# Performance work log

Hardware: AMD Instinct MI355X
Metric: run time of the kernel (lower is better)

Reference implementation:

```python
import jax, jax.numpy as jnp
import numpy as np

SIGMA = 0.02
B, CC, H, W = 4, 21, 96, 96
C_LOW, C_HIGH = 3, 512
N = H * W


def _grid_edges(h, w):
    idx = np.arange(h * w).reshape(h, w)
    eh = np.stack([idx[:, :-1].ravel(), idx[:, 1:].ravel()], 1)
    ev = np.stack([idx[:-1, :].ravel(), idx[1:, :].ravel()], 1)
    return np.concatenate([eh, ev], 0)  # [E,2] 4-connected grid edges


def _mst_bfs(feat, h, w):
    # feat: [C,h,w] numpy. Kruskal MST with norm2 edge weights, then BFS from node 0.
    n = h * w
    edges = _grid_edges(h, w)
    f = feat.reshape(feat.shape[0], -1)
    wts = ((f[:, edges[:, 0]] - f[:, edges[:, 1]]) ** 2).sum(0)
    order = np.argsort(wts, kind='stable')
    uf = np.arange(n)

    def find(x):
        r = x
        while uf[r] != r:
            r = uf[r]
        while uf[x] != r:
            uf[x], x = r, uf[x]
        return r

    adj = [[] for _ in range(n)]
    cnt = 0
    for ei in order:
        a, b = int(edges[ei, 0]), int(edges[ei, 1])
        ra, rb = find(a), find(b)
        if ra != rb:
            uf[ra] = rb
            adj[a].append(b)
            adj[b].append(a)
            cnt += 1
            if cnt == n - 1:
                break
    parent = np.zeros(n, np.int64)
    seen = np.zeros(n, bool)
    seen[0] = True
    levels, frontier = [[0]], [0]
    while frontier:
        nxt = []
        for u in frontier:
            for v in adj[u]:
                if not seen[v]:
                    seen[v] = True
                    parent[v] = u
                    nxt.append(v)
        if nxt:
            levels.append(nxt)
        frontier = nxt
    return parent, levels


def _tree_arrays(embed):
    # Host-side MST + BFS level schedule (integer tree topology, non-differentiable).
    e = np.asarray(jax.device_get(embed)).astype(np.float64)
    bn = e.shape[0]
    parents, levels = [], []
    for b in range(bn):
        p, lv = _mst_bfs(e[b], H, W)
        parents.append(p)
        levels.append(lv)
    D = max(len(lv) for lv in levels)
    L = max(max(len(l) for l in lv) for lv in levels)
    nodes = np.full((bn, D, L), N, np.int32)  # index N = dummy sink node
    for b, lv in enumerate(levels):
        for d, l in enumerate(lv):
            nodes[b, d, :len(l)] = l
    par = np.stack(parents)
    par = np.concatenate([par, np.full((bn, 1), N)], 1).astype(np.int32)
    msk = np.ones((bn, N + 1), np.float32)
    msk[:, 0] = 0.0  # root has no parent edge
    msk[:, N] = 0.0  # dummy node
    return jnp.asarray(nodes), jnp.asarray(par), jnp.asarray(msk)


def _tree_filter(feat, embed, nodes, parent, wmask, sigma):
    # feat [B,C,N], embed [B,Ce,N]. O(N) two-pass (leaf->root, root->leaf) tree DP:
    # out_i = sum_j (prod_{e in path(i,j)} w_e) f_j / same-with-f=1
    bn, c, nn = feat.shape
    ez = jnp.pad(embed, ((0, 0), (0, 0), (0, 1)))  # add dummy column
    ep = jax.vmap(lambda e, p: e[:, p])(ez, parent)  # parent embedding [B,Ce,N+1]
    w = wmask * jnp.exp(-((ez - ep) ** 2).sum(1) / sigma)  # edge weight per node [B,N+1]
    fa = jnp.concatenate([feat, jnp.ones((bn, 1, nn), feat.dtype)], 1)  # append norm channel
    fa = jnp.pad(fa, ((0, 0), (0, 0), (0, 1)))  # [B,C+1,N+1]

    def one(a0, wv, par, lvls):
        def up(a, lvl):  # children before parents: subtree aggregation
            return a.at[:, par[lvl]].add(wv[lvl] * a[:, lvl]), None
        a, _ = jax.lax.scan(up, a0, lvls[::-1])

        def down(s, lvl):  # parents before children: whole-tree aggregation
            wl = wv[lvl]
            sv = a[:, lvl] + wl * (s[:, par[lvl]] - wl * a[:, lvl])
            return s.at[:, lvl].set(sv), None
        s, _ = jax.lax.scan(down, a, lvls)
        return s

    s = jax.vmap(one)(fa, w, parent, nodes)
    return s[:, :c, :nn] / s[:, c:, :nn]


def _nearest(x, h, w):
    hr, wr = x.shape[-2:]
    ri = jnp.arange(h) * hr // h
    ci = jnp.arange(w) * wr // w
    return x[..., ri[:, None], ci[None, :]]


def setup_inputs():
    key = jax.random.key(0)
    k1, k2, k3, k4 = jax.random.split(key, 4)
    preds = jax.random.normal(k1, (B, CC, H, W), jnp.float32)
    low_feats = jax.random.uniform(k2, (B, C_LOW, H, W), dtype=jnp.float32)
    high_feats = 0.03 * jax.random.normal(k3, (B, C_HIGH, H, W), jnp.float32)
    roi = (jax.random.uniform(k4, (B, 1, 2 * H, 2 * W)) > 0.5).astype(jnp.float32)
    return {'preds': preds, 'low_feats': low_feats, 'high_feats': high_feats,
            'unlabeled_ROIs': roi}


def reference(preds, low_feats, high_feats, unlabeled_ROIs):
    nodes_l, par_l, msk_l = _tree_arrays(low_feats)
    nodes_h, par_h, msk_h = _tree_arrays(high_feats)
    roi = _nearest(unlabeled_ROIs, H, W)
    n = roi.sum()
    prob = jax.nn.sigmoid(preds)
    lf = low_feats.reshape(B, C_LOW, N)
    hf = high_feats.reshape(B, C_HIGH, N)
    AS = _tree_filter(prob.reshape(B, CC, N), lf, nodes_l, par_l, msk_l, SIGMA)
    AS = _tree_filter(AS, hf, nodes_h, par_h, msk_h, 1.0)
    loss = (roi * jnp.abs(prob - AS.reshape(B, CC, H, W))).sum()
    return jnp.where(n > 0, loss / n, jnp.zeros_like(loss))
```

## Files before the change

kernel.cpp:

```cpp
#include <hip/hip_runtime.h>
#include <math.h>
#include <stdint.h>
#include <stddef.h>


namespace {
constexpr int Bn  = 4, Cc = 21, Hh = 96, Ww = 96;
constexpr int Nn  = Hh * Ww;
constexpr int EhE = Hh * (Ww - 1);
constexpr int Ne  = EhE + (Hh - 1) * Ww;
constexpr int Clow = 3, Chigh = 512;
constexpr int NCh = Cc + 1;
constexpr int MAXD = 2048;
constexpr int TL  = 2 * (Nn - 1);
constexpr int ESL = 18432;
constexpr int SEG = 19;
constexpr int NR  = (TL + SEG - 1) / SEG;
constexpr int MAXC = 4608;

constexpr size_t OFF_ACC  = 0;
constexpr size_t OFF_PROB = 256;
constexpr size_t OFF_S1   = OFF_PROB + (size_t)Bn * Cc * Nn * 4;
constexpr size_t OFF_S2   = OFF_S1   + (size_t)Bn * NCh * Nn * 4;
constexpr size_t OFF_EW   = OFF_S2   + (size_t)Bn * NCh * Nn * 4;
constexpr size_t OFF_ORD  = OFF_EW   + (size_t)8 * Ne * 8;
constexpr size_t OFF_PPOS = OFF_ORD  + (size_t)8 * Nn * 4;
constexpr size_t OFF_WGT  = OFF_PPOS + (size_t)8 * Nn * 2;
constexpr size_t OFF_LEV  = OFF_WGT  + (size_t)8 * Nn * 4;
constexpr size_t OFF_D    = OFF_LEV  + (size_t)8 * MAXD * 4;
constexpr size_t OFF_DIR  = OFF_D    + 256;
constexpr size_t OFF_CBW  = OFF_DIR  + (size_t)8 * Nn * 4;
constexpr size_t OFF_CBE  = OFF_CBW  + (size_t)8 * Nn * 8;
constexpr size_t OFF_OPP  = OFF_CBE  + (size_t)8 * Nn * 4;
constexpr size_t OFF_SGN  = OFF_OPP  + (size_t)8 * ESL * 2;
constexpr size_t OFF_PNF  = OFF_SGN  + (size_t)8 * ESL;
constexpr size_t OFF_RNK  = OFF_PNF  + (size_t)8 * Nn * 4;
constexpr size_t OFF_EL1  = OFF_ORD;
constexpr size_t OFF_EL2  = OFF_WGT;
}

__device__ __forceinline__ void edge_nodes(int e, int& a, int& b) {
    if (e < EhE) { int h = e / (Ww - 1), w = e - h * (Ww - 1); a = h * Ww + w; b = a + 1; }
    else { int e2 = e - EhE; int h = e2 / Ww, w = e2 - h * Ww; a = h * Ww + w; b = a + Ww; }
}
__device__ __forceinline__ int dir_delta(int d) {
    return (d == 0) ? 1 : (d == 1) ? -1 : (d == 2) ? Ww : -Ww;
}
__device__ __forceinline__ int edge_of(int u, int d) {
    int h = u / Ww, w = u - h * Ww;
    if (d == 0) return h * (Ww - 1) + w;
    if (d == 1) return h * (Ww - 1) + w - 1;
    if (d == 2) return EhE + u;
    return EhE + u - Ww;
}

__device__ __forceinline__ unsigned long long mkkey(double w, int e) {
    unsigned long long q = (unsigned long long)(w * 70368744177664.0);
    if (q >= (1ull << 49)) q = (1ull << 49) - 1;
    return (q << 15) | (unsigned)e;
}

__device__ __forceinline__ void compact_push(bool keep, int val, int* cnt,
                                             unsigned short* out, int lane) {
    unsigned long long m = __ballot(keep ? 1 : 0);
    if (m == 0ull) return;
    int leader = __ffsll((unsigned long long)m) - 1;
    int base = 0;
    if (lane == leader) base = atomicAdd(cnt, __popcll(m));
    base = __shfl(base, leader, 64);
    if (keep) {
        unsigned long long lower = m & ((1ull << lane) - 1ull);
        out[base + __popcll(lower)] = (unsigned short)val;
    }
}

__device__ __forceinline__ int scan1024s(int val, int tid, int* wsum) {
    __syncthreads();
    int lane = tid & 63, wv = tid >> 6;
    int x = val;
    #pragma unroll
    for (int off = 1; off < 64; off <<= 1) {
        int y = __shfl_up(x, off, 64);
        if (lane >= off) x += y;
    }
    if (lane == 63) wsum[wv] = x;
    __syncthreads();
    if (wv == 0) {
        int s2 = (lane < 16) ? wsum[lane] : 0;
        #pragma unroll
        for (int off = 1; off < 16; off <<= 1) {
            int y = __shfl_up(s2, off, 64);
            if (lane >= off) s2 += y;
        }
        if (lane < 16) wsum[lane] = s2;
    }
    __syncthreads();
    int base = (wv > 0) ? wsum[wv - 1] : 0;
    return x + base;
}

__device__ __forceinline__ int scan1024_incl(int val, int tid, int* b0, int* b1) {
    b0[tid] = val;
    __syncthreads();
    int* s = b0; int* d = b1;
    for (int off = 1; off < 1024; off <<= 1) {
        int x = s[tid];
        if (tid >= off) x += s[tid - off];
        d[tid] = x;
        __syncthreads();
        int* t = s; s = d; d = t;
    }
    return s[tid];
}

__global__ void k_init(const float* __restrict__ preds, float* __restrict__ prob,
                       double* __restrict__ acc) {
    int idx = blockIdx.x * blockDim.x + threadIdx.x;
    if (idx == 0) { acc[0] = 0.0; acc[1] = 0.0; }
    if (idx >= Bn * Cc * Nn) return;
    prob[idx] = 1.0f / (1.0f + expf(-preds[idx]));
}

__global__ void k_edgew(const float* __restrict__ feat, int C, double* __restrict__ ew) {
    int idx = blockIdx.x * blockDim.x + threadIdx.x;
    if (idx >= Bn * Ne) return;
    int b = idx / Ne, e = idx - b * Ne;
    int a, c2; edge_nodes(e, a, c2);
    const float* fa = feat + (size_t)b * C * Nn + a;
    const float* fb = feat + (size_t)b * C * Nn + c2;
    double s = 0.0;
    int c = 0;
    for (; c + 16 <= C; c += 16) {
        float va[16], vb[16];
        #pragma unroll
        for (int k = 0; k < 16; k++) {
            va[k] = fa[(size_t)(c + k) * Nn];
            vb[k] = fb[(size_t)(c + k) * Nn];
        }
        #pragma unroll
        for (int k = 0; k < 16; k++) {
            double d = (double)va[k] - (double)vb[k];
            s += d * d;
        }
    }
    for (; c < C; c++) {
        double d = (double)fa[(size_t)c * Nn] - (double)fb[(size_t)c * Nn];
        s += d * d;
    }
    ew[idx] = s;
}

__global__ void __launch_bounds__(1024)
k_mst(char* __restrict__ ws) {
    const int tb = blockIdx.x, tid = threadIdx.x;
    const int lane = tid & 63;
    const double* ew = (const double*)(ws + OFF_EW) + (size_t)tb * Ne;
    int* dirG = (int*)(ws + OFF_DIR) + (size_t)tb * Nn;
    unsigned short* elA = (unsigned short*)(ws + OFF_EL1) + (size_t)tb * Ne;
    unsigned short* elB = (unsigned short*)(ws + OFF_EL2) + (size_t)tb * Ne;

    __shared__ unsigned short comp[Nn];
    __shared__ unsigned long long cbK[MAXC];
    __shared__ int scanBuf[2048];
    __shared__ int chgArr[48];
    __shared__ int sLen, sNC;

    unsigned short* nxtN     = (unsigned short*)cbK;
    unsigned short* newSlotN = (unsigned short*)cbK + Nn;
    unsigned short* nxt      = (unsigned short*)cbK;
    unsigned short* newSlot  = (unsigned short*)cbK + MAXC;

    for (int i = tid; i < Nn; i += 1024) dirG[i] = 0;
    if (tid < 48) chgArr[tid] = 0;
    __syncthreads();

    for (int i = tid; i < Nn; i += 1024) {
        int h = i / Ww, w = i - h * Ww;
        unsigned long long bk = ~0ull;
        if (w < Ww - 1) { int e = h * (Ww - 1) + w;     unsigned long long k = mkkey(ew[e], e); if (k < bk) bk = k; }
        if (w > 0)      { int e = h * (Ww - 1) + w - 1; unsigned long long k = mkkey(ew[e], e); if (k < bk) bk = k; }
        if (h < Hh - 1) { int e = EhE + i;              unsigned long long k = mkkey(ew[e], e); if (k < bk) bk = k; }
        if (h > 0)      { int e = EhE + i - Ww;         unsigned long long k = mkkey(ew[e], e); if (k < bk) bk = k; }
        int e = (int)(bk & 0x7FFF);
        int a, c; edge_nodes(e, a, c);
        nxtN[i] = (unsigned short)((a == i) ? c : a);
        int da = (c == a + 1) ? 0 : 2;
        atomicOr(&dirG[a], 1 << da);
        atomicOr(&dirG[c], 1 << (da ^ 1));
    }
    __syncthreads();
    for (int i = tid; i < Nn; i += 1024) {
        int o = nxtN[i];
        if (o != i && nxtN[o] == i && i < o) nxtN[i] = (unsigned short)i;
    }
    __syncthreads();
    {
        int it = 0;
        while (it < 40) {
            bool any = false;
            for (int r = tid; r < Nn; r += 1024) {
                int nr = nxtN[r], nnr = nxtN[nr];
                if (nr != nnr) { nxtN[r] = (unsigned short)nnr; any = true; }
            }
            if (any) chgArr[it] = 1;
            __syncthreads();
            if (!chgArr[it]) break;
            it++;
        }
    }
    {
        int base = tid * 9, cnt = 0, loc[9];
        #pragma unroll
        for (int k = 0; k < 9; k++) {
            int i = base + k;
            loc[k] = cnt;
            if (nxtN[i] == i) cnt++;
        }
        int incl = scan1024_incl(cnt, tid, scanBuf, scanBuf + 1024);
        int eb = incl - cnt;
        #pragma unroll
        for (int k = 0; k < 9; k++) {
            int i = base + k;
            if (nxtN[i] == i) newSlotN[i] = (unsigned short)(eb + loc[k]);
        }
        if (tid == 1023) sNC = incl;
    }
    __syncthreads();
    for (int i = tid; i < Nn; i += 1024) comp[i] = newSlotN[nxtN[i]];
    __syncthreads();
    int nComp = sNC;

    unsigned short* src = elA;
    unsigned short* dst = elB;
    int srcLen = -1;
    for (int round = 2; round < 22 && nComp > 1; round++) {
        if (tid == 0) sLen = 0;
        if (tid < 48) chgArr[tid] = 0;
        __syncthreads();
        if (srcLen < 0) {
            for (int e = tid; e < Ne; e += 1024) {
                int a, c; edge_nodes(e, a, c);
                compact_push(comp[a] != comp[c], e, &sLen, dst, lane);
            }
        } else {
            for (int k = tid; k < srcLen; k += 1024) {
                int e = src[k];
                int a, c; edge_nodes(e, a, c);
                compact_push(comp[a] != comp[c], e, &sLen, dst, lane);
            }
        }
        for (int s = tid; s < nComp; s += 1024) cbK[s] = ~0ull;
        __syncthreads();
        int len = sLen;
        if (len == 0) break;
        for (int k = tid; k < len; k += 1024) {
            int e = dst[k];
            int a, c; edge_nodes(e, a, c);
            unsigned long long key = mkkey(ew[e], e);
            atomicMin(&cbK[comp[a]], key);
            atomicMin(&cbK[comp[c]], key);
        }
        __syncthreads();
        unsigned long long kr[5];
        int nOwn = 0;
        for (int s = tid; s < nComp; s += 1024) kr[nOwn++] = cbK[s];
        __syncthreads();
        {
            int o = 0;
            for (int s = tid; s < nComp; s += 1024, o++) {
                unsigned long long key = kr[o];
                if (key != ~0ull) {
                    int e = (int)(key & 0x7FFF);
                    int a, c; edge_nodes(e, a, c);
                    int sa = comp[a], sc = comp[c];
                    nxt[s] = (unsigned short)((sa == s) ? sc : sa);
                    int da = (c == a + 1) ? 0 : 2;
                    atomicOr(&dirG[a], 1 << da);
                    atomicOr(&dirG[c], 1 << (da ^ 1));
                } else nxt[s] = (unsigned short)s;
            }
        }
        __syncthreads();
        for (int s = tid; s < nComp; s += 1024) {
            int o = nxt[s];
            if (o != s && nxt[o] == s && s < o) nxt[s] = (unsigned short)s;
        }
        __syncthreads();
        {
            int it = 0;
            while (it < 40) {
                bool any = false;
                for (int s = tid; s < nComp; s += 1024) {
                    int ns = nxt[s], nns = nxt[ns];
                    if (ns != nns) { nxt[s] = (unsigned short)nns; any = true; }
                }
                if (any) chgArr[it] = 1;
                __syncthreads();
                if (!chgArr[it]) break;
                it++;
            }
        }
        {
            int K = (nComp + 1023) >> 10;
            int base = tid * K, cnt = 0, loc[5];
            for (int k = 0; k < K; k++) {
                int s = base + k;
                loc[k] = cnt;
                if (s < nComp && nxt[s] == s) cnt++;
            }
            int incl = scan1024_incl(cnt, tid, scanBuf, scanBuf + 1024);
            int eb = incl - cnt;
            for (int k = 0; k < K; k++) {
                int s = base + k;
                if (s < nComp && nxt[s] == s) newSlot[s] = (unsigned short)(eb + loc[k]);
            }
            if (tid == 1023) sNC = incl;
        }
        __syncthreads();
        for (int i = tid; i < Nn; i += 1024) comp[i] = newSlot[nxt[comp[i]]];
        __syncthreads();
        nComp = sNC;
        unsigned short* t = src; src = dst; dst = t;
        srcLen = len;
    }
}

__global__ void __launch_bounds__(1024)
k_topo(char* __restrict__ ws) {
    const int tb = blockIdx.x, tid = threadIdx.x;
    const int lane = tid & 63, wv = tid >> 6;
    const int tree = tb >> 2;
    const double* ew  = (const double*)(ws + OFF_EW) + (size_t)tb * Ne;
    const int*  dirG  = (const int*)(ws + OFF_DIR) + (size_t)tb * Nn;
    unsigned int*   elemSegG = (unsigned int*)(ws + OFF_CBW + (size_t)tb * 73728);
    unsigned short* ORG      = (unsigned short*)(ws + OFF_CBW + (size_t)tb * 73728);
    unsigned short* OWNR     = ORG + ESL;
    unsigned short* ownG     = (unsigned short*)(ws + OFF_CBE + (size_t)tb * (size_t)ESL * 2);
    unsigned short* oppG     = (unsigned short*)(ws + OFF_OPP + (size_t)tb * (size_t)ESL * 2);
    unsigned short* IRG      = (unsigned short*)(ws + OFF_SGN + (size_t)tb * ESL);
    unsigned short* rank0G   = (unsigned short*)(ws + OFF_RNK + (size_t)tb * (size_t)ESL * 2);
    int*            ordG  = (int*)(ws + OFF_ORD)  + (size_t)tb * Nn;
    unsigned short* pposG = (unsigned short*)(ws + OFF_PPOS) + (size_t)tb * Nn;
    float*          wgtG  = (float*)(ws + OFF_WGT) + (size_t)tb * Nn;
    int*            levG  = (int*)(ws + OFF_LEV)  + (size_t)tb * MAXD;
    int*            dG    = (int*)(ws + OFF_D);
    const float inv_sigma = tree ? 1.0f : 50.0f;

    __shared__ char A[36864];
    __shared__ char B[18432];
    __shared__ char C[9216];
    __shared__ int  wsum[16];
    __shared__ int  sR, sPack, sCenter;

    unsigned short* degOff = (unsigned short*)B;
    unsigned char*  nbS    = (unsigned char*)C;
    for (int i = tid; i < Nn; i += 1024) nbS[i] = (unsigned char)dirG[i];
    __syncthreads();
    {
        int base9 = tid * 9;
        int loc[9]; int s = 0;
        #pragma unroll
        for (int k = 0; k < 9; k++) { loc[k] = s; s += __popc(nbS[base9 + k]); }
        int incl = scan1024s(s, tid, wsum);
        int eb = incl - s;
        #pragma unroll
        for (int k = 0; k < 9; k++) degOff[base9 + k] = (unsigned short)(eb + loc[k]);
    }
    __syncthreads();

    unsigned short* nxtS = (unsigned short*)A;
    for (int u = tid; u < Nn; u += 1024) {
        int m = nbS[u]; int base = degOff[u]; int k = 0;
        #pragma unroll
        for (int d = 0; d < 4; d++) {
            if (m & (1 << d)) {
                int v = u + dir_delta(d);
                int mv = nbS[v]; int rd = d ^ 1;
                int pv = __popc(mv & ((1 << rd) - 1));
                int dv = __popc(mv);
                int nx = pv + 1; if (nx == dv) nx = 0;
                int j = base + k;
                nxtS[j] = (unsigned short)(degOff[v] + nx);
                ownG[j] = (unsigned short)((u << 2) | d);
                oppG[j] = (unsigned short)(degOff[v] + pv);
                k++;
            }
        }
    }
    __syncthreads();

    int myNr = 0, myLen = 0;
    if (tid < NR) {
        int x = tid * SEG, off = 0;
        for (int g = 0; g < 4096; g++) {
            elemSegG[x] = ((unsigned)tid << 11) | (unsigned)off;
            int y = nxtS[x];
            if (y % SEG == 0) { myNr = y / SEG; myLen = off + 1; break; }
            x = y; off++;
        }
    }
    __syncthreads();

    unsigned short* cn  = (unsigned short*)C;
    unsigned short* cd  = (unsigned short*)(C + 2048);
    unsigned short* nn2 = (unsigned short*)(C + 4096);
    unsigned short* nd2 = (unsigned short*)(C + 6144);
    if (tid == 0)      { cn[0] = 0; cd[0] = 0; }
    else if (tid < NR) { cn[tid] = (unsigned short)myNr; cd[tid] = (unsigned short)myLen; }
    else               { cn[tid] = (unsigned short)tid; cd[tid] = 0; }
    __syncthreads();
    for (int r = 0; r < 10; r++) {
        int c = cn[tid];
        int dv = cd[tid] + cd[c];
        int n2 = cn[c];
        nn2[tid] = (unsigned short)n2; nd2[tid] = (unsigned short)dv;
        __syncthreads();
        unsigned short* t;
        t = cn; cn = nn2; nn2 = t;
        t = cd; cd = nd2; nd2 = t;
    }
    unsigned short* rb = nn2;
    rb[tid] = (tid == 0) ? 0 : (unsigned short)(TL - cd[tid]);
    __syncthreads();

    for (int e = tid; e < TL; e += 1024) {
        unsigned int pk = elemSegG[e];
        rank0G[e] = (unsigned short)(rb[pk >> 11] + (pk & 2047));
    }
    __syncthreads();

    for (int j = tid; j < TL; j += 1024) {
        int r = rank0G[j];
        ORG[r]  = rank0G[oppG[j]];
        OWNR[r] = ownG[j];
    }
    for (int x = tid; x < Nn; x += 1024)
        IRG[x] = rank0G[oppG[degOff[x]]];
    __syncthreads();

    short* scanS = (short*)A;
    unsigned char* parC = (unsigned char*)C;
    unsigned short* depthB = (unsigned short*)B;
    int curRoot = 0, rootC = 0;
    for (int ph = 0; ph < 3; ph++) {
        if (tid == 0) {
            sR = ORG[IRG[curRoot]];
            sPack = 0;
        }
        __syncthreads();
        const int R = sR;
        const bool doPar = (ph >= 1);
        int base = tid * 18;
        int n = TL - base; if (n > 18) n = 18; if (n < 0) n = 0;
        short loc[18]; int s = 0;
        for (int k = 0; k < n; k++) {
            int q = base + k;
            int r = q + R; if (r >= TL) r -= TL;
            int orv = ORG[r];
            int rro = orv - R; if (rro < 0) rro += TL;
            bool desc = q < rro;
            if (doPar && desc) {
                int own = OWNR[r];
                int head = (own >> 2) + dir_delta(own & 3);
                parC[head] = (unsigned char)((own & 3) ^ 1);
            }
            s += desc ? 1 : -1;
            loc[k] = (short)s;
        }
        int incl = scan1024s(s, tid, wsum);
        int eb = incl - s;
        for (int k = 0; k < n; k++) scanS[base + k] = (short)(loc[k] + eb);
        __syncthreads();
        int pk = 0;
        for (int x = tid; x < Nn; x += 1024) {
            int q = IRG[x] - R; if (q < 0) q += TL;
            int dep = (x == curRoot) ? 0 : (int)scanS[q];
            int p2 = (dep << 14) | x;
            if (p2 > pk) pk = p2;
            if (ph == 2) depthB[x] = (unsigned short)dep;
        }
        #pragma unroll
        for (int off = 32; off > 0; off >>= 1) {
            int o = __shfl_down(pk, off, 64);
            if (o > pk) pk = o;
        }
        if (lane == 0) atomicMax(&sPack, pk);
        __syncthreads();
        if (ph == 0) curRoot = sPack & 16383;
        else if (ph == 1) {
            if (tid == 0) {
                int diam = sPack >> 14, v = sPack & 16383;
                int steps = diam - (diam >> 1);
                int x = v;
                for (int k2 = 0; k2 < steps; k2++) x += dir_delta(parC[x]);
                sCenter = x;
            }
            __syncthreads();
            curRoot = sCenter;
            rootC = curRoot;
        }
        __syncthreads();
    }
    const int D = (sPack >> 14) + 1;

    unsigned short* posOf = (unsigned short*)A;
    int* hist   = (int*)(A + 18432);
    int* levOff = (int*)(A + 26624);
    for (int k = tid; k < 2048; k += 1024) hist[k] = 0;
    __syncthreads();
    for (int v = tid; v < Nn; v += 1024) atomicAdd(&hist[depthB[v]], 1);
    __syncthreads();
    {
        int h0 = hist[2 * tid], h1 = hist[2 * tid + 1];
        int partial = h0 + h1;
        int incl = scan1024s(partial, tid, wsum);
        int eb = incl - partial;
        levOff[2 * tid] = eb;
        levOff[2 * tid + 1] = eb + h0;
    }
    __syncthreads();
    for (int d = tid; d <= D && d < 2048; d += 1024) levG[d] = levOff[d];
    for (int k = tid; k < 2048; k += 1024) hist[k] = 0;
    __syncthreads();
    for (int v = tid; v < Nn; v += 1024) {
        int dep = depthB[v];
        int pos = levOff[dep] + atomicAdd(&hist[dep], 1);
        posOf[v] = (unsigned short)pos;
        ordG[pos] = v;
    }
    __syncthreads();

    for (int v = tid; v < Nn; v += 1024) {
        int pos = posOf[v];
        if (v == rootC) { pposG[pos] = 0; wgtG[pos] = 0.0f; }
        else {
            int rd = parC[v];
            int p = v + dir_delta(rd);
            pposG[pos] = posOf[p];
            wgtG[pos] = expf(-(float)ew[edge_of(v, rd)] * inv_sigma);
        }
    }
    if (tid == 0) dG[tb] = D;
}

__global__ void __launch_bounds__(64)
k_dp(char* __restrict__ ws, int tree, int inMode) {
    const int bc = blockIdx.x;
    const int b = bc / NCh, c = bc % NCh;
    const int tb = tree * Bn + b;
    const int lane = threadIdx.x;
    const int*            ordG  = (const int*)(ws + OFF_ORD)  + (size_t)tb * Nn;
    const unsigned short* pposG = (const unsigned short*)(ws + OFF_PPOS) + (size_t)tb * Nn;
    const float*          wgtG  = (const float*)(ws + OFF_WGT) + (size_t)tb * Nn;
    const int*            levG  = (const int*)(ws + OFF_LEV)  + (size_t)tb * MAXD;
    const int D = ((const int*)(ws + OFF_D))[tb];
    const float* src = (inMode == 0)
        ? (const float*)(ws + OFF_PROB) + ((size_t)b * Cc + c) * Nn
        : (const float*)(ws + OFF_S1)   + ((size_t)b * NCh + c) * Nn;
    const float* srcN = (const float*)(ws + OFF_S1) + ((size_t)b * NCh + Cc) * Nn;
    float* dst = (float*)(ws + (tree ? OFF_S2 : OFF_S1)) + ((size_t)b * NCh + c) * Nn;

    __shared__ alignas(16) float Al[Nn];
    __shared__ alignas(16) float wgtS[Nn];
    __shared__ alignas(16) unsigned short pposS[Nn];
    __shared__ unsigned short levS[MAXD];

    {
        const uint4* pg4 = (const uint4*)pposG;
        uint4* ps4 = (uint4*)pposS;
        for (int k = lane; k < Nn / 8; k += 64) ps4[k] = pg4[k];
        const uint4* wg4 = (const uint4*)wgtG;
        uint4* ws4 = (uint4*)wgtS;
        for (int k = lane; k < Nn / 4; k += 64) ws4[k] = wg4[k];
    }
    for (int d = lane; d <= D && d < MAXD; d += 64) levS[d] = (unsigned short)levG[d];
    if (c == Cc)            { for (int i = lane; i < Nn; i += 64) Al[i] = 1.0f; }
    else if (inMode == 0)   { for (int i = lane; i < Nn; i += 64) Al[i] = src[ordG[i]]; }
    else                    { for (int i = lane; i < Nn; i += 64) { int nd = ordG[i]; Al[i] = src[nd] / srcN[nd]; } }
    __builtin_amdgcn_wave_barrier();
    asm volatile("" ::: "memory");

    if (D > 1) {
        int sd = levS[D - 1], sd1 = levS[D];
        for (int d = D - 1; d >= 1; d--) {
            int nb = (d > 1) ? (int)levS[d - 1] : 0;
            for (int i = sd + lane; i < sd1; i += 64)
                atomicAdd(&Al[pposS[i]], wgtS[i] * Al[i]);
            __builtin_amdgcn_wave_barrier();
            asm volatile("" ::: "memory");
            sd1 = sd; sd = nb;
        }
    }
    if (D > 1) {
        int sd = levS[1], sd1 = levS[2];
        for (int d = 1; d < D; d++) {
            int nb = (d + 2 <= D) ? (int)levS[d + 2] : 0;
            for (int i = sd + lane; i < sd1; i += 64) {
                float w = wgtS[i], a = Al[i];
                Al[i] = a + w * (Al[pposS[i]] - w * a);
            }
            __builtin_amdgcn_wave_barrier();
            asm volatile("" ::: "memory");
            sd = sd1; sd1 = nb;
        }
    }
    __builtin_amdgcn_wave_barrier();
    asm volatile("" ::: "memory");
    for (int i = lane; i < Nn; i += 64) dst[ordG[i]] = Al[i];
}

__global__ void k_loss(char* __restrict__ ws, const float* __restrict__ roi) {
    const int tid = threadIdx.x;
    int idx = blockIdx.x * 256 + tid;
    const float* prob = (const float*)(ws + OFF_PROB);
    const float* S2   = (const float*)(ws + OFF_S2);
    double* acc = (double*)(ws + OFF_ACC);
    double ls = 0.0, cnt = 0.0;
    if (idx < Bn * Cc * Nn) {
        int b = idx / (Cc * Nn);
        int rem = idx - b * (Cc * Nn);
        int c = rem / Nn, n = rem - c * Nn;
        int h = n / Ww, w2 = n - h * Ww;
        float r = roi[(size_t)b * (2 * Hh) * (2 * Ww) + (size_t)(2 * h) * (2 * Ww) + 2 * w2];
        float as = S2[((size_t)b * NCh + c) * Nn + n] / S2[((size_t)b * NCh + Cc) * Nn + n];
        float pp = prob[((size_t)b * Cc + c) * Nn + n];
        ls = (double)(r * fabsf(pp - as));
        if (c == 0) cnt = (double)r;
    }
    __shared__ double sl[256], sc2[256];
    sl[tid] = ls; sc2[tid] = cnt;
    __syncthreads();
    for (int s = 128; s > 0; s >>= 1) {
        if (tid < s) { sl[tid] += sl[tid + s]; sc2[tid] += sc2[tid + s]; }
        __syncthreads();
    }
    if (tid == 0) { atomicAdd(acc, sl[0]); atomicAdd(acc + 1, sc2[0]); }
}

__global__ void k_final(const double* __restrict__ acc, float* __restrict__ out) {
    if (blockIdx.x == 0 && threadIdx.x == 0)
        out[0] = (acc[1] > 0.0) ? (float)(acc[0] / acc[1]) : 0.0f;
}

extern "C" void kernel_launch(void* const* d_in, const int* in_sizes, int n_in,
                              void* d_out, int out_size, void* d_ws, size_t ws_size,
                              hipStream_t stream) {
    const float* preds = (const float*)d_in[0];
    const float* lowf  = (const float*)d_in[1];
    const float* highf = (const float*)d_in[2];
    const float* roi   = (const float*)d_in[3];
    char* ws = (char*)d_ws;
    float* out = (float*)d_out;
    double* ewl = (double*)(ws + OFF_EW);
    double* ewh = (double*)(ws + OFF_EW) + (size_t)Bn * Ne;

    k_init<<<(Bn * Cc * Nn + 255) / 256, 256, 0, stream>>>(
        preds, (float*)(ws + OFF_PROB), (double*)(ws + OFF_ACC));
    k_edgew<<<(Bn * Ne + 255) / 256, 256, 0, stream>>>(lowf, Clow, ewl);
    k_edgew<<<(Bn * Ne + 255) / 256, 256, 0, stream>>>(highf, Chigh, ewh);
    k_mst<<<8, 1024, 0, stream>>>(ws);
    k_topo<<<8, 1024, 0, stream>>>(ws);
    k_dp<<<Bn * NCh, 64, 0, stream>>>(ws, 0, 0);
    k_dp<<<Bn * NCh, 64, 0, stream>>>(ws, 1, 1);
    k_loss<<<(Bn * Cc * Nn + 255) / 256, 256, 0, stream>>>(ws, roi);
    k_final<<<1, 64, 0, stream>>>((const double*)(ws + OFF_ACC), out);
}
```

Baseline: 719.4 us.

## Batch gathers in tree-build kernel and parallelize center walk via pointer jumping

Strided gather loops in the tree-construction kernel are rewritten into unrolled, batched register arrays, so that many independent loads go out before their results are used. This is meant to hide memory latency. The serial single-thread walk up the parent chain to find the tree center is replaced by block-wide pointer jumping (binary lifting) in shared memory. That turns a long dependent chain into a logarithmic number of synchronized rounds. The cost is more register pressure and extra barriers per doubling round.

New measurement: 670.1 us. -6.9%, faster.

```diff
diff --git a/kernel.cpp b/kernel.cpp
--- a/kernel.cpp
+++ b/kernel.cpp
@@ -423,19 +423,54 @@
     rb[tid] = (tid == 0) ? 0 : (unsigned short)(TL - cd[tid]);
     __syncthreads();
 
-    for (int e = tid; e < TL; e += 1024) {
-        unsigned int pk = elemSegG[e];
-        rank0G[e] = (unsigned short)(rb[pk >> 11] + (pk & 2047));
-    }
-    __syncthreads();
-
-    for (int j = tid; j < TL; j += 1024) {
-        int r = rank0G[j];
-        ORG[r]  = rank0G[oppG[j]];
-        OWNR[r] = ownG[j];
-    }
-    for (int x = tid; x < Nn; x += 1024)
-        IRG[x] = rank0G[oppG[degOff[x]]];
+    for (int hh = 0; hh < 2; hh++) {
+        unsigned int pk4[9];
+        #pragma unroll
+        for (int t = 0; t < 9; t++) {
+            int e = tid + (hh * 9 + t) * 1024;
+            pk4[t] = elemSegG[e < TL ? e : 0];
+        }
+        unsigned short rbv[9];
+        #pragma unroll
+        for (int t = 0; t < 9; t++) rbv[t] = rb[pk4[t] >> 11];
+        #pragma unroll
+        for (int t = 0; t < 9; t++) {
+            int e = tid + (hh * 9 + t) * 1024;
+            if (e < TL) rank0G[e] = (unsigned short)(rbv[t] + (pk4[t] & 2047));
+        }
+    }
+    __syncthreads();
+
+    for (int hh = 0; hh < 2; hh++) {
+        unsigned short rnk[9], opp[9], own2[9];
+        #pragma unroll
+        for (int t = 0; t < 9; t++) {
+            int j = tid + (hh * 9 + t) * 1024;
+            int ja = j < TL ? j : 0;
+            rnk[t] = rank0G[ja]; opp[t] = oppG[ja]; own2[t] = ownG[ja];
+        }
+        unsigned short r2[9];
+        #pragma unroll
+        for (int t = 0; t < 9; t++) r2[t] = rank0G[opp[t]];
+        #pragma unroll
+        for (int t = 0; t < 9; t++) {
+            int j = tid + (hh * 9 + t) * 1024;
+            if (j < TL) { int r = rnk[t]; ORG[r] = r2[t]; OWNR[r] = own2[t]; }
+        }
+    }
+    {
+        unsigned short dof[9];
+        #pragma unroll
+        for (int t = 0; t < 9; t++) dof[t] = degOff[tid + t * 1024];
+        unsigned short ov[9];
+        #pragma unroll
+        for (int t = 0; t < 9; t++) ov[t] = oppG[dof[t]];
+        unsigned short rv[9];
+        #pragma unroll
+        for (int t = 0; t < 9; t++) rv[t] = rank0G[ov[t]];
+        #pragma unroll
+        for (int t = 0; t < 9; t++) IRG[tid + t * 1024] = rv[t];
+    }
     __syncthreads();
 
     short* scanS = (short*)A;
@@ -452,32 +487,62 @@
         const bool doPar = (ph >= 1);
         int base = tid * 18;
         int n = TL - base; if (n > 18) n = 18; if (n < 0) n = 0;
+        unsigned short orvA[18], ownA[18];
+        #pragma unroll
+        for (int k = 0; k < 18; k++) {
+            int q = base + k;
+            int r = q + R; if (r >= TL) r -= TL; if (q >= TL) r = 0;
+            orvA[k] = ORG[r];
+        }
+        if (doPar) {
+            #pragma unroll
+            for (int k = 0; k < 18; k++) {
+                int q = base + k;
+                int r = q + R; if (r >= TL) r -= TL; if (q >= TL) r = 0;
+                ownA[k] = OWNR[r];
+            }
+        }
         short loc[18]; int s = 0;
-        for (int k = 0; k < n; k++) {
-            int q = base + k;
-            int r = q + R; if (r >= TL) r -= TL;
-            int orv = ORG[r];
-            int rro = orv - R; if (rro < 0) rro += TL;
-            bool desc = q < rro;
-            if (doPar && desc) {
-                int own = OWNR[r];
-                int head = (own >> 2) + dir_delta(own & 3);
-                parC[head] = (unsigned char)((own & 3) ^ 1);
-            }
-            s += desc ? 1 : -1;
-            loc[k] = (short)s;
+        #pragma unroll
+        for (int k = 0; k < 18; k++) {
+            if (k < n) {
+                int q = base + k;
+                int rro = (int)orvA[k] - R; if (rro < 0) rro += TL;
+                bool desc = q < rro;
+                if (doPar && desc) {
+                    int own = ownA[k];
+                    int head = (own >> 2) + dir_delta(own & 3);
+                    parC[head] = (unsigned char)((own & 3) ^ 1);
+                }
+                s += desc ? 1 : -1;
+                loc[k] = (short)s;
+            }
         }
         int incl = scan1024s(s, tid, wsum);
         int eb = incl - s;
-        for (int k = 0; k < n; k++) scanS[base + k] = (short)(loc[k] + eb);
+        #pragma unroll
+        for (int k = 0; k < 18; k++)
+            if (k < n) scanS[base + k] = (short)(loc[k] + eb);
         __syncthreads();
         int pk = 0;
-        for (int x = tid; x < Nn; x += 1024) {
-            int q = IRG[x] - R; if (q < 0) q += TL;
-            int dep = (x == curRoot) ? 0 : (int)scanS[q];
-            int p2 = (dep << 14) | x;
-            if (p2 > pk) pk = p2;
-            if (ph == 2) depthB[x] = (unsigned short)dep;
+        {
+            unsigned short qA[9];
+            #pragma unroll
+            for (int j = 0; j < 9; j++) qA[j] = IRG[tid + j * 1024];
+            int depA[9];
+            #pragma unroll
+            for (int j = 0; j < 9; j++) {
+                int q = (int)qA[j] - R; if (q < 0) q += TL;
+                depA[j] = (int)scanS[q];
+            }
+            #pragma unroll
+            for (int j = 0; j < 9; j++) {
+                int x = tid + j * 1024;
+                int dep = (x == curRoot) ? 0 : depA[j];
+                int p2 = (dep << 14) | x;
+                if (p2 > pk) pk = p2;
+                if (ph == 2) depthB[x] = (unsigned short)dep;
+            }
         }
         #pragma unroll
         for (int off = 32; off > 0; off >>= 1) {
@@ -488,12 +553,22 @@
         __syncthreads();
         if (ph == 0) curRoot = sPack & 16383;
         else if (ph == 1) {
-            if (tid == 0) {
-                int diam = sPack >> 14, v = sPack & 16383;
-                int steps = diam - (diam >> 1);
-                int x = v;
-                for (int k2 = 0; k2 < steps; k2++) x += dir_delta(parC[x]);
-                sCenter = x;
+            int diam = sPack >> 14, v = sPack & 16383;
+            int steps = diam - (diam >> 1);
+            unsigned short* J  = (unsigned short*)A;
+            unsigned short* J2 = (unsigned short*)(A + 18432);
+            for (int x = tid; x < Nn; x += 1024)
+                J[x] = (unsigned short)((x == curRoot) ? x : (x + dir_delta(parC[x])));
+            if (tid == 0) sCenter = v;
+            __syncthreads();
+            for (int k = 0; (steps >> k) != 0; k++) {
+                if (tid == 0 && ((steps >> k) & 1)) sCenter = J[sCenter];
+                if ((steps >> (k + 1)) != 0) {
+                    __syncthreads();
+                    for (int x = tid; x < Nn; x += 1024) J2[x] = J[J[x]];
+                    __syncthreads();
+                    unsigned short* t = J; J = J2; J2 = t;
+                }
             }
             __syncthreads();
             curRoot = sCenter;
@@ -530,14 +605,33 @@
     }
     __syncthreads();
 
-    for (int v = tid; v < Nn; v += 1024) {
-        int pos = posOf[v];
-        if (v == rootC) { pposG[pos] = 0; wgtG[pos] = 0.0f; }
-        else {
-            int rd = parC[v];
-            int p = v + dir_delta(rd);
-            pposG[pos] = posOf[p];
-            wgtG[pos] = expf(-(float)ew[edge_of(v, rd)] * inv_sigma);
+    {
+        unsigned char rdA[9]; unsigned short posA[9];
+        #pragma unroll
+        for (int t = 0; t < 9; t++) {
+            int v = tid + t * 1024;
+            rdA[t] = parC[v]; posA[t] = posOf[v];
+        }
+        double ewv[9]; unsigned short ppv[9];
+        #pragma unroll
+        for (int t = 0; t < 9; t++) {
+            int v = tid + t * 1024;
+            int rd = rdA[t] & 3;
+            bool ir = (v == rootC);
+            int p  = ir ? v : v + dir_delta(rd);
+            int ei = ir ? 0 : edge_of(v, rd);
+            ppv[t] = posOf[p];
+            ewv[t] = ew[ei];
+        }
+        #pragma unroll
+        for (int t = 0; t < 9; t++) {
+            int v = tid + t * 1024;
+            int pos = posA[t];
+            if (v == rootC) { pposG[pos] = 0; wgtG[pos] = 0.0f; }
+            else {
+                pposG[pos] = ppv[t];
+                wgtG[pos] = expf(-(float)ewv[t] * inv_sigma);
+            }
         }
     }
     if (tid == 0) dG[tb] = D;
```
